# Kernel tuning notes

Hardware: AMD Instinct MI355X
Metric: run time of the kernel (lower is better)

Reference implementation:

```python
import jax, jax.numpy as jnp
import numpy as np

B, S, D = 2, 2048, 1024
H, DK = 16, 64
NUM_BUCKETS, MAX_DIST = 32, 128
EPS = 1e-6


def _relative_position_bucket(q_len, k_len):
    # T5 bidirectional relative position bucketing.
    ctx = jnp.arange(q_len)[:, None]
    mem = jnp.arange(k_len)[None, :]
    rel = mem - ctx  # [q, k]
    nb = NUM_BUCKETS // 2
    ret = (rel > 0).astype(jnp.int32) * nb
    n = jnp.abs(rel)
    max_exact = nb // 2
    is_small = n < max_exact
    n_safe = jnp.maximum(n, 1).astype(jnp.float32)
    val_large = max_exact + (
        jnp.log(n_safe / max_exact) / np.log(MAX_DIST / max_exact) * (nb - max_exact)
    ).astype(jnp.int32)
    val_large = jnp.minimum(val_large, nb - 1)
    return ret + jnp.where(is_small, n, val_large)  # [q, k] int32


def setup_inputs() -> dict:
    key = jax.random.key(0)
    ks = jax.random.split(key, 7)
    s = 0.02
    return {
        "hidden_states": jax.random.normal(ks[0], (B, S, D), jnp.float32),
        "ln_g": jnp.ones((D,), jnp.float32),
        "ln_b": jnp.zeros((D,), jnp.float32),
        "Wq": jax.random.normal(ks[1], (D, H * DK), jnp.float32) * s,
        "Wk": jax.random.normal(ks[2], (D, H * DK), jnp.float32) * s,
        "Wv": jax.random.normal(ks[3], (D, H * DK), jnp.float32) * s,
        "Wo": jax.random.normal(ks[4], (H * DK, D), jnp.float32) * s,
        "rel_bias": jax.random.normal(ks[5], (NUM_BUCKETS, H), jnp.float32) * s,
    }


def reference(hidden_states, ln_g, ln_b, Wq, Wk, Wv, Wo, rel_bias):
    b, s, d = hidden_states.shape
    # LayerNorm (nn.LayerNorm with affine, biased variance)
    mu = jnp.mean(hidden_states, axis=-1, keepdims=True)
    var = jnp.mean(jnp.square(hidden_states - mu), axis=-1, keepdims=True)
    normed = (hidden_states - mu) * jax.lax.rsqrt(var + EPS) * ln_g + ln_b
    # QKV projections (no bias), split heads
    q = (normed @ Wq).reshape(b, s, H, DK)
    k = (normed @ Wk).reshape(b, s, H, DK)
    v = (normed @ Wv).reshape(b, s, H, DK)
    # T5 attention: NO 1/sqrt(d) scaling; learned relative-position bias added to logits
    scores = jnp.einsum("bqhd,bkhd->bhqk", q, k)
    bucket = _relative_position_bucket(s, s)          # [s, s]
    bias = jnp.transpose(rel_bias[bucket], (2, 0, 1))  # [H, s, s]
    attn = jax.nn.softmax(scores + bias[None], axis=-1)
    ctx = jnp.einsum("bhqk,bkhd->bqhd", attn, v).reshape(b, s, H * DK)
    out = ctx @ Wo
    # residual (dropout is identity in eval)
    return hidden_states + out
```

## Files before the change

### kernel.cpp

```cpp
#include <hip/hip_runtime.h>
#include <hip/hip_bf16.h>
#include <math.h>

typedef __attribute__((__ext_vector_type__(8))) short bf16x8;
typedef __attribute__((__ext_vector_type__(4))) float f32x4;
typedef __attribute__((__ext_vector_type__(16))) float f32x16;
typedef __attribute__((__ext_vector_type__(4))) unsigned int u32x4;

#define B_ 2
#define S_ 2048
#define D_ 1024
#define H_ 16
#define DK_ 64
#define M_ (B_*S_)
#define N3_ 3072
#define BIAS_LEN 4096
#define M0_ 24.0f
#define L2E_ 1.4426950408889634f
#define KSTRIDE 66

__device__ __forceinline__ unsigned int cvtpk(float a, float b){
  unsigned int r;
  asm("v_cvt_pk_bf16_f32 %0, %1, %2" : "=v"(r) : "v"(a), "v"(b));
  return r;
}
__device__ __forceinline__ unsigned short f2bf(float f){
  unsigned int r;
  asm("v_cvt_pk_bf16_f32 %0, %1, %2" : "=v"(r) : "v"(f), "v"(f));
  return (unsigned short)r;
}
__device__ __forceinline__ float bf2f(unsigned short u){
  union{unsigned int i; float f;} v; v.i = ((unsigned int)u)<<16; return v.f;
}

__device__ __forceinline__ float fexp2(float x){
#if __has_builtin(__builtin_amdgcn_exp2f)
  return __builtin_amdgcn_exp2f(x);
#else
  return __expf(x * 0.6931471805599453f);
#endif
}

__device__ __forceinline__ f32x4 zero4(){
  f32x4 z; z[0]=0.f; z[1]=0.f; z[2]=0.f; z[3]=0.f; return z;
}

__device__ __forceinline__ f32x4 mfma16(bf16x8 a, bf16x8 b, f32x4 c){
  return __builtin_amdgcn_mfma_f32_16x16x32_bf16(a, b, c, 0, 0, 0);
}
__device__ __forceinline__ f32x16 mfma32(bf16x8 a, bf16x8 b, f32x16 c){
  return __builtin_amdgcn_mfma_f32_32x32x16_bf16(a, b, c, 0, 0, 0);
}

__device__ __forceinline__ void gload16(const void* g, void* l){
  __builtin_amdgcn_global_load_lds(
      (const __attribute__((address_space(1))) void*)g,
      (__attribute__((address_space(3))) void*)l, 16, 0, 0);
}

__global__ __launch_bounds__(256) void transpose_cast_kernel(
    const float* __restrict__ Wq, const float* __restrict__ Wk,
    const float* __restrict__ Wv, const float* __restrict__ Wo,
    unsigned short* __restrict__ Wcat_t, unsigned short* __restrict__ Wo_t)
{
  __shared__ float tile[64][65];
  const int k0 = blockIdx.x * 64;
  const int v0 = blockIdx.y * 64;
  const int sel = v0 >> 10;
  const float* W = (sel==0) ? Wq : (sel==1) ? Wk : (sel==2) ? Wv : Wo;
  const int nn0 = v0 & 1023;
  #pragma unroll
  for (int i=0;i<16;i++){
    int idx = i*256 + threadIdx.x;
    int r = idx >> 6, c = idx & 63;
    tile[r][c] = W[(size_t)(k0+r)*1024 + nn0 + c];
  }
  __syncthreads();
  #pragma unroll
  for (int i=0;i<16;i++){
    int idx = i*256 + threadIdx.x;
    int nr = idx >> 6, kc = idx & 63;
    unsigned short bv = f2bf(tile[kc][nr]);
    if (sel < 3) Wcat_t[(size_t)(v0+nr)*1024 + k0 + kc] = bv;
    else         Wo_t[(size_t)(v0-3072+nr)*1024 + k0 + kc] = bv;
  }
}

__global__ __launch_bounds__(256) void bias_tab_kernel(
    const float* __restrict__ rel_bias, float* __restrict__ biasTab)
{
  int t = blockIdx.x*256 + threadIdx.x;
  if (t >= H_*BIAS_LEN) return;
  int h = t / BIAS_LEN;
  int idx = t - h*BIAS_LEN;
  int rel = idx - (S_-1);
  int ret = (rel > 0) ? 16 : 0;
  int n = (rel < 0) ? -rel : rel;
  int bidx;
  if (n < 8) bidx = n;
  else {
    float vl = logf((float)n * 0.125f) / 2.7725887f * 8.0f;
    int v = 8 + (int)vl;
    bidx = (v < 15) ? v : 15;
  }
  biasTab[t] = (rel_bias[(ret + bidx)*H_ + h] - M0_) * L2E_;
}

__global__ __launch_bounds__(256) void ln_kernel(
    const float* __restrict__ x, const float* __restrict__ g,
    const float* __restrict__ bta, unsigned short* __restrict__ out)
{
  const int row = blockIdx.x;
  const int tid = threadIdx.x;
  float4 v = ((const float4*)(x + (size_t)row*D_))[tid];
  float s  = v.x+v.y+v.z+v.w;
  float ss = v.x*v.x+v.y*v.y+v.z*v.z+v.w*v.w;
  #pragma unroll
  for (int off=1; off<64; off<<=1){ s += __shfl_xor(s,off,64); ss += __shfl_xor(ss,off,64); }
  __shared__ float rs[4], rss[4];
  const int wid = tid >> 6, lane = tid & 63;
  if (lane == 0){ rs[wid] = s; rss[wid] = ss; }
  __syncthreads();
  s  = rs[0]+rs[1]+rs[2]+rs[3];
  ss = rss[0]+rss[1]+rss[2]+rss[3];
  float mu  = s * (1.0f/1024.0f);
  float var = ss * (1.0f/1024.0f) - mu*mu;
  float rstd = rsqrtf(var + 1e-6f);
  float4 gg = ((const float4*)g)[tid];
  float4 bb = ((const float4*)bta)[tid];
  uint2 o;
  o.x = cvtpk((v.x-mu)*rstd*gg.x + bb.x, (v.y-mu)*rstd*gg.y + bb.y);
  o.y = cvtpk((v.z-mu)*rstd*gg.z + bb.z, (v.w-mu)*rstd*gg.w + bb.w);
  ((uint2*)(out + (size_t)row*D_))[tid] = o;
}

__global__ __launch_bounds__(256) void gemm_qkv_kernel(
    const unsigned short* __restrict__ A,
    const unsigned short* __restrict__ Bt,
    unsigned short* __restrict__ Qb,
    unsigned short* __restrict__ Kb,
    unsigned short* __restrict__ Vtb)
{
  __shared__ unsigned short As[128*64];
  __shared__ unsigned short Bs[128*64];
  const int tid = threadIdx.x;
  const int wid = tid >> 6, lane = tid & 63;
  const int lr = lane & 15, lg = lane >> 4;
  const int wm = (wid >> 1) * 64, wn = (wid & 1) * 64;

  const int nbx = gridDim.x;
  const int total = nbx * gridDim.y;
  const int flat = blockIdx.y * nbx + blockIdx.x;
  const int swz = (flat & 7) * (total >> 3) + (flat >> 3);
  const int m0 = (swz % nbx) * 128, n0 = (swz / nbx) * 128;

  f32x4 acc[4][4];
  #pragma unroll
  for (int i=0;i<4;i++)
    #pragma unroll
    for (int j=0;j<4;j++) acc[i][j] = zero4();

  for (int k0 = 0; k0 < D_; k0 += 64) {
    __syncthreads();
    #pragma unroll
    for (int i=0;i<4;i++){
      int c = i*256 + tid;
      int row = c >> 3, ch = c & 7;
      int chs = ch ^ (row & 7);
      gload16(A  + (size_t)(m0+row)*D_ + k0 + chs*8, As + c*8);
      gload16(Bt + (size_t)(n0+row)*D_ + k0 + chs*8, Bs + c*8);
    }
    __syncthreads();
    #pragma unroll
    for (int kk=0;kk<2;kk++){
      bf16x8 aF[4], bF[4];
      #pragma unroll
      for (int mi=0;mi<4;mi++){
        int row = wm + mi*16 + lr;
        aF[mi] = *(const bf16x8*)&As[row*64 + (((kk*4+lg) ^ (row & 7)) * 8)];
      }
      #pragma unroll
      for (int ni=0;ni<4;ni++){
        int row = wn + ni*16 + lr;
        bF[ni] = *(const bf16x8*)&Bs[row*64 + (((kk*4+lg) ^ (row & 7)) * 8)];
      }
      #pragma unroll
      for (int mi=0;mi<4;mi++)
        #pragma unroll
        for (int ni=0;ni<4;ni++)
          acc[mi][ni] = mfma16(aF[mi], bF[ni], acc[mi][ni]);
    }
  }

  const int seln = n0 >> 10;
  if (seln == 2) {
    #pragma unroll
    for (int mi=0;mi<4;mi++)
      #pragma unroll
      for (int ni=0;ni<4;ni++){
        int m = m0 + wm + mi*16 + lg*4;
        int n = n0 + wn + ni*16 + lr;
        int nn = n & 1023, hh = nn >> 6, dk = nn & 63;
        int b = m >> 11, s = m & 2047;
        uint2 u;
        u.x = cvtpk(acc[mi][ni][0], acc[mi][ni][1]);
        u.y = cvtpk(acc[mi][ni][2], acc[mi][ni][3]);
        *(uint2*)(Vtb + (((size_t)(b*H_+hh))*DK_ + dk)*S_ + s) = u;
      }
  } else {
    unsigned short* __restrict__ dst = (seln == 0) ? Qb : Kb;
    #pragma unroll
    for (int mi=0;mi<4;mi++)
      #pragma unroll
      for (int ni=0;ni<4;ni++)
        #pragma unroll
        for (int r=0;r<4;r++){
          int m = m0 + wm + mi*16 + lg*4 + r;
          int n = n0 + wn + ni*16 + lr;
          int nn = n & 1023, hh = nn >> 6, dk = nn & 63;
          int b = m >> 11, s = m & 2047;
          dst[(((size_t)(b*H_+hh))*S_ + s)*DK_ + dk] = f2bf(acc[mi][ni][r]);
        }
  }
}

#define SOFTMAX_PV(Svec, BG, UNIP, UNIN, VF00, VF01, VF10, VF11, ACC, LS)        \
{                                                                                \
  float p[16];                                                                   \
  if (UNIP) {                                                                    \
    _Pragma("unroll")                                                            \
    for (int r=0;r<16;r++) p[r] = fexp2(__builtin_fmaf(Svec[r], L2E_, cpos));    \
  } else if (UNIN) {                                                             \
    _Pragma("unroll")                                                            \
    for (int r=0;r<16;r++) p[r] = fexp2(__builtin_fmaf(Svec[r], L2E_, cneg));    \
  } else {                                                                       \
    _Pragma("unroll")                                                            \
    for (int r=0;r<16;r++){                                                      \
      int key = k0 + st*32 + (r&3) + 8*(r>>2) + 4*hi;                            \
      p[r] = fexp2(__builtin_fmaf(Svec[r], L2E_, BG[key]));                      \
    }                                                                            \
  }                                                                              \
                                       \
  {                                                                              \
    float t0=p[0]+p[1], t1=p[2]+p[3], t2=p[4]+p[5], t3=p[6]+p[7];                \
    float t4=p[8]+p[9], t5=p[10]+p[11], t6=p[12]+p[13], t7=p[14]+p[15];          \
    LS += ((t0+t1)+(t2+t3)) + ((t4+t5)+(t6+t7));                                 \
  }                                                                              \
  unsigned int W00=cvtpk(p[0],p[1]),  W01=cvtpk(p[4],p[5]);                      \
  unsigned int W02=cvtpk(p[8],p[9]),  W03=cvtpk(p[12],p[13]);                    \
  unsigned int W10=cvtpk(p[2],p[3]),  W11=cvtpk(p[6],p[7]);                      \
  unsigned int W12=cvtpk(p[10],p[11]),W13=cvtpk(p[14],p[15]);                    \
  unsigned int X00=__shfl_xor(W00,32), X01=__shfl_xor(W01,32);                   \
  unsigned int X02=__shfl_xor(W02,32), X03=__shfl_xor(W03,32);                   \
  unsigned int X10=__shfl_xor(W10,32), X11=__shfl_xor(W11,32);                   \
  unsigned int X12=__shfl_xor(W12,32), X13=__shfl_xor(W13,32);                   \
  u32x4 pu0; u32x4 pu1;                                                          \
  pu0[0] = hi ? X01 : W00;  pu0[1] = hi ? X11 : W10;                             \
  pu0[2] = hi ? W01 : X00;  pu0[3] = hi ? W11 : X10;                             \
  pu1[0] = hi ? X03 : W02;  pu1[1] = hi ? X13 : W12;                             \
  pu1[2] = hi ? W03 : X02;  pu1[3] = hi ? W13 : X12;                             \
  bf16x8 pav0 = __builtin_bit_cast(bf16x8, pu0);                                 \
  bf16x8 pav1 = __builtin_bit_cast(bf16x8, pu1);                                 \
  ACC[0] = mfma32(pav0, VF00, ACC[0]);                                           \
  ACC[1] = mfma32(pav0, VF01, ACC[1]);                                           \
  ACC[0] = mfma32(pav1, VF10, ACC[0]);                                           \
  ACC[1] = mfma32(pav1, VF11, ACC[1]);                                           \
}

__global__ __launch_bounds__(256, 2) void attn_kernel(
    const unsigned short* __restrict__ Qb,
    const unsigned short* __restrict__ Kb,
    const unsigned short* __restrict__ Vtb,
    const float* __restrict__ biasTab,
    const float* __restrict__ rel_bias,
    unsigned short* __restrict__ Opart,
    float* __restrict__ Lpart)
{
  __shared__ unsigned short Ks[64*KSTRIDE];
  __shared__ unsigned short Vts[64*KSTRIDE];

  const int tid = threadIdx.x;
  const int wid = tid >> 6, lane = tid & 63;
  const int ql = lane & 31;
  const int hi = lane >> 5;

  const int flat = (blockIdx.z * 32 + blockIdx.y) * 8 + blockIdx.x;
  const int wf = (flat & 7) * 64 + (flat >> 3);
  const int qt = wf & 7;
  const int bh = (wf >> 3) & 31;
  const int kg = wf >> 8;

  const int h = bh & (H_-1);
  const int b = bh >> 4;
  const int kbase = kg << 10;
  const int q0w = qt*256 + wid*64;

  const float cpos = (rel_bias[31*H_ + h] - M0_) * L2E_;
  const float cneg = (rel_bias[15*H_ + h] - M0_) * L2E_;
  const float* bGa = biasTab + (size_t)h*BIAS_LEN + 2047 - (q0w + ql);
  const float* bGb = bGa - 32;

  const unsigned short* Qpa = Qb + ((size_t)bh*S_ + q0w + ql)*DK_;
  bf16x8 qfa[4], qfb[4];
  #pragma unroll
  for (int c=0;c<4;c++){
    qfa[c] = *(const bf16x8*)(Qpa + 16*c + 8*hi);
    qfb[c] = *(const bf16x8*)(Qpa + 32*DK_ + 16*c + 8*hi);
  }

  const unsigned short* Ksrc = Kb  + (size_t)bh*S_*DK_;
  const unsigned short* Vsrc = Vtb + (size_t)bh*DK_*S_;
  const int c0 = tid, c1 = tid + 256;
  const int r0 = c0 >> 3, ch0 = c0 & 7;
  const int r1 = c1 >> 3, ch1 = c1 & 7;

  f32x16 acca[2], accb[2];
  #pragma unroll
  for (int i=0;i<16;i++){ acca[0][i]=0.f; acca[1][i]=0.f; accb[0][i]=0.f; accb[1][i]=0.f; }
  float lsa = 0.f, lsb = 0.f;

  bf16x8 sk0 = *(const bf16x8*)(Ksrc + (size_t)(kbase + r0)*DK_ + ch0*8);
  bf16x8 sk1 = *(const bf16x8*)(Ksrc + (size_t)(kbase + r1)*DK_ + ch1*8);
  bf16x8 sv0 = *(const bf16x8*)(Vsrc + (size_t)r0*S_ + kbase + ch0*8);
  bf16x8 sv1 = *(const bf16x8*)(Vsrc + (size_t)r1*S_ + kbase + ch1*8);

  for (int k0 = kbase; k0 < kbase + 1024; k0 += 64) {
    __syncthreads();
    *(bf16x8*)&Ks [r0*KSTRIDE + ch0*8] = sk0;
    *(bf16x8*)&Ks [r1*KSTRIDE + ch1*8] = sk1;
    *(bf16x8*)&Vts[r0*KSTRIDE + ch0*8] = sv0;
    *(bf16x8*)&Vts[r1*KSTRIDE + ch1*8] = sv1;
    __syncthreads();
    if (k0 + 64 < kbase + 1024) {
      int kn = k0 + 64;
      sk0 = *(const bf16x8*)(Ksrc + (size_t)(kn + r0)*DK_ + ch0*8);
      sk1 = *(const bf16x8*)(Ksrc + (size_t)(kn + r1)*DK_ + ch1*8);
      sv0 = *(const bf16x8*)(Vsrc + (size_t)r0*S_ + kn + ch0*8);
      sv1 = *(const bf16x8*)(Vsrc + (size_t)r1*S_ + kn + ch1*8);
    }

    const bool upa = (k0 >= q0w + 122),      una = (k0 <= q0w - 154);
    const bool upb = (k0 >= q0w + 32 + 122), unb = (k0 <= q0w + 32 - 154);

    #pragma unroll
    for (int st=0; st<2; ++st){
      const int arow = st*32 + ql;
      bf16x8 kf0 = *(const bf16x8*)&Ks[arow*KSTRIDE + (0+hi)*8];
      bf16x8 kf1 = *(const bf16x8*)&Ks[arow*KSTRIDE + (2+hi)*8];
      bf16x8 kf2 = *(const bf16x8*)&Ks[arow*KSTRIDE + (4+hi)*8];
      bf16x8 kf3 = *(const bf16x8*)&Ks[arow*KSTRIDE + (6+hi)*8];

      f32x16 sa, sb;
      #pragma unroll
      for (int i=0;i<16;i++){ sa[i]=0.f; sb[i]=0.f; }
      sa = mfma32(kf0, qfa[0], sa); sb = mfma32(kf0, qfb[0], sb);
      sa = mfma32(kf1, qfa[1], sa); sb = mfma32(kf1, qfb[1], sb);
      sa = mfma32(kf2, qfa[2], sa); sb = mfma32(kf2, qfb[2], sb);
      sa = mfma32(kf3, qfa[3], sa); sb = mfma32(kf3, qfb[3], sb);

      bf16x8 vf00 = *(const bf16x8*)&Vts[(ql     )*KSTRIDE + (4*st+  hi)*8];
      bf16x8 vf01 = *(const bf16x8*)&Vts[(ql + 32)*KSTRIDE + (4*st+  hi)*8];
      bf16x8 vf10 = *(const bf16x8*)&Vts[(ql     )*KSTRIDE + (4*st+2+hi)*8];
      bf16x8 vf11 = *(const bf16x8*)&Vts[(ql + 32)*KSTRIDE + (4*st+2+hi)*8];

      SOFTMAX_PV(sa, bGa, upa, una, vf00, vf01, vf10, vf11, acca, lsa);
      SOFTMAX_PV(sb, bGb, upb, unb, vf00, vf01, vf10, vf11, accb, lsb);
    }
  }

  float lta = lsa + __shfl_xor(lsa, 32);
  float ltb = lsb + __shfl_xor(lsb, 32);
  if (hi == 0) {
    Lpart[((size_t)kg*B_*H_ + bh)*S_ + q0w + ql]      = lta;
    Lpart[((size_t)kg*B_*H_ + bh)*S_ + q0w + 32 + ql] = ltb;
  }
  #pragma unroll
  for (int r=0;r<16;r++){
    const int qr = (r&3) + 8*(r>>2) + 4*hi;
    #pragma unroll
    for (int dt=0; dt<2; ++dt){
      const int d = ql + 32*dt;
      Opart[(size_t)kg*M_*D_ + ((size_t)(b*S_ + q0w + qr)*H_ + h)*DK_ + d]      = f2bf(acca[dt][r]);
      Opart[(size_t)kg*M_*D_ + ((size_t)(b*S_ + q0w + 32 + qr)*H_ + h)*DK_ + d] = f2bf(accb[dt][r]);
    }
  }
}

__global__ __launch_bounds__(256) void gemm_out_kernel(
    const unsigned short* __restrict__ Opart,
    const float* __restrict__ Lpart,
    const unsigned short* __restrict__ Wo_t,
    const float* __restrict__ resid,
    float* __restrict__ outf)
{
  __shared__ unsigned short As[64*64];
  __shared__ unsigned short Bs[128*64];
  const int tid = threadIdx.x;
  const int wid = tid >> 6, lane = tid & 63;
  const int lr = lane & 15, lg = lane >> 4;
  const int wm = (wid & 1) * 32, wn = (wid >> 1) * 64;

  const int nbx = gridDim.x;
  const int total = nbx * gridDim.y;
  const int flat = blockIdx.y * nbx + blockIdx.x;
  const int swz = (flat & 7) * (total >> 3) + (flat >> 3);
  const int m0 = (swz % nbx) * 64, n0 = (swz / nbx) * 128;

  f32x4 acc[2][4];
  #pragma unroll
  for (int i=0;i<2;i++)
    #pragma unroll
    for (int j=0;j<4;j++) acc[i][j] = zero4();

  for (int k0 = 0; k0 < D_; k0 += 64) {
    const int hh = k0 >> 6;
    __syncthreads();
    #pragma unroll
    for (int i=0;i<4;i++){
      int c = i*256 + tid;
      int row = c >> 3, ch = c & 7;
      int chs = ch ^ (row & 7);
      gload16(Wo_t + (size_t)(n0+row)*D_ + k0 + chs*8, Bs + c*8);
    }
    #pragma unroll
    for (int i=0;i<2;i++){
      int c = i*256 + tid;
      int row = c >> 3, ch = c & 7;
      int m = m0 + row;
      int bb = m >> 11, s = m & 2047;
      int bhh = bb*H_ + hh;
      float l0 = Lpart[(size_t)bhh*S_ + s];
      float l1 = Lpart[(size_t)B_*H_*S_ + (size_t)bhh*S_ + s];
      float li = 1.0f / (l0 + l1);
      size_t addr = (size_t)m*D_ + k0 + ch*8;
      bf16x8 p0 = *(const bf16x8*)(Opart + addr);
      bf16x8 p1 = *(const bf16x8*)(Opart + (size_t)M_*D_ + addr);
      u32x4 o;
      #pragma unroll
      for (int j=0;j<4;j++){
        float a = (bf2f((unsigned short)p0[2*j+0]) + bf2f((unsigned short)p1[2*j+0])) * li;
        float cc= (bf2f((unsigned short)p0[2*j+1]) + bf2f((unsigned short)p1[2*j+1])) * li;
        o[j] = cvtpk(a, cc);
      }
      *(u32x4*)&As[row*64 + ((ch ^ (row & 7))*8)] = o;
    }
    __syncthreads();
    #pragma unroll
    for (int kk=0;kk<2;kk++){
      bf16x8 aF[2], bF[4];
      #pragma unroll
      for (int mi=0;mi<2;mi++){
        int row = wm + mi*16 + lr;
        aF[mi] = *(const bf16x8*)&As[row*64 + (((kk*4+lg) ^ (row & 7)) * 8)];
      }
      #pragma unroll
      for (int ni=0;ni<4;ni++){
        int row = wn + ni*16 + lr;
        bF[ni] = *(const bf16x8*)&Bs[row*64 + (((kk*4+lg) ^ (row & 7)) * 8)];
      }
      #pragma unroll
      for (int mi=0;mi<2;mi++)
        #pragma unroll
        for (int ni=0;ni<4;ni++)
          acc[mi][ni] = mfma16(aF[mi], bF[ni], acc[mi][ni]);
    }
  }

  #pragma unroll
  for (int mi=0;mi<2;mi++)
    #pragma unroll
    for (int ni=0;ni<4;ni++)
      #pragma unroll
      for (int r=0;r<4;r++){
        int m = m0 + wm + mi*16 + lg*4 + r;
        int n = n0 + wn + ni*16 + lr;
        outf[(size_t)m*D_ + n] = acc[mi][ni][r] + resid[(size_t)m*D_ + n];
      }
}

extern "C" void kernel_launch(void* const* d_in, const int* in_sizes, int n_in,
                              void* d_out, int out_size, void* d_ws, size_t ws_size,
                              hipStream_t stream) {
  const float* hidden   = (const float*)d_in[0];
  const float* ln_g     = (const float*)d_in[1];
  const float* ln_b     = (const float*)d_in[2];
  const float* Wq       = (const float*)d_in[3];
  const float* Wk       = (const float*)d_in[4];
  const float* Wv       = (const float*)d_in[5];
  const float* Wo       = (const float*)d_in[6];
  const float* rel_bias = (const float*)d_in[7];
  float* out = (float*)d_out;

  char* ws = (char*)d_ws;
  const size_t off_ln   = 0;
  const size_t off_wcat = 8388608;
  const size_t off_q    = 16777216;
  const size_t off_k    = 25165824;
  const size_t off_vt   = 33554432;
  const size_t off_bias = 50331648;
  const size_t off_lp   = 50593792;
  const size_t off_wo   = 51118080;

  unsigned short* ln_out  = (unsigned short*)(ws + off_ln);
  unsigned short* Wcat_t  = (unsigned short*)(ws + off_wcat);
  unsigned short* Wo_t    = (unsigned short*)(ws + off_wo);
  unsigned short* Qb      = (unsigned short*)(ws + off_q);
  unsigned short* Kb      = (unsigned short*)(ws + off_k);
  unsigned short* Vtb     = (unsigned short*)(ws + off_vt);
  float*          biasTab = (float*)(ws + off_bias);
  float*          Lpart   = (float*)(ws + off_lp);
  unsigned short* Opart   = (unsigned short*)(ws + 0);

  transpose_cast_kernel<<<dim3(16,64), 256, 0, stream>>>(Wq, Wk, Wv, Wo, Wcat_t, Wo_t);
  bias_tab_kernel<<<(H_*BIAS_LEN + 255)/256, 256, 0, stream>>>(rel_bias, biasTab);
  ln_kernel<<<M_, 256, 0, stream>>>(hidden, ln_g, ln_b, ln_out);
  gemm_qkv_kernel<<<dim3(M_/128, N3_/128), 256, 0, stream>>>(
      ln_out, Wcat_t, Qb, Kb, Vtb);
  attn_kernel<<<dim3(8, 32, 2), 256, 0, stream>>>(
      Qb, Kb, Vtb, biasTab, rel_bias, Opart, Lpart);
  gemm_out_kernel<<<dim3(M_/64, D_/128), 256, 0, stream>>>(
      Opart, Lpart, Wo_t, hidden, out);
}
```

Baseline: 140.6 us.

## Double-buffer K/V in LDS and optionally split attention keys four ways

Attention now keeps two LDS buffers for K and V tiles. The next tile is written while the current one is consumed, so each iteration needs one barrier instead of two. The key dimension split is templated: if the workspace is large enough, it uses four key partitions (double the blocks) and gemm_out sums four partials. This adds more partial-output traffic in bf16 and relies on ws_size to choose the path.

```diff
diff --git a/kernel.cpp b/kernel.cpp
--- a/kernel.cpp
+++ b/kernel.cpp
@@ -267,6 +267,7 @@
   ACC[1] = mfma32(pav1, VF11, ACC[1]);                                           \
 }
 
+template<int NS>
 __global__ __launch_bounds__(256, 2) void attn_kernel(
     const unsigned short* __restrict__ Qb,
     const unsigned short* __restrict__ Kb,
@@ -276,8 +277,10 @@
     unsigned short* __restrict__ Opart,
     float* __restrict__ Lpart)
 {
-  __shared__ unsigned short Ks[64*KSTRIDE];
-  __shared__ unsigned short Vts[64*KSTRIDE];
+  __shared__ unsigned short Ks[2][64*KSTRIDE];
+  __shared__ unsigned short Vts[2][64*KSTRIDE];
+  constexpr int NT = (S_/NS)/64;
+  constexpr int KSPAN = S_/NS;
 
   const int tid = threadIdx.x;
   const int wid = tid >> 6, lane = tid & 63;
@@ -285,14 +288,14 @@
   const int hi = lane >> 5;
 
   const int flat = (blockIdx.z * 32 + blockIdx.y) * 8 + blockIdx.x;
-  const int wf = (flat & 7) * 64 + (flat >> 3);
+  const int wf = (flat & 7) * (32 * NS) + (flat >> 3);
   const int qt = wf & 7;
   const int bh = (wf >> 3) & 31;
   const int kg = wf >> 8;
 
   const int h = bh & (H_-1);
   const int b = bh >> 4;
-  const int kbase = kg << 10;
+  const int kbase = kg * KSPAN;
   const int q0w = qt*256 + wid*64;
 
   const float cpos = (rel_bias[31*H_ + h] - M0_) * L2E_;
@@ -323,21 +326,24 @@
   bf16x8 sk1 = *(const bf16x8*)(Ksrc + (size_t)(kbase + r1)*DK_ + ch1*8);
   bf16x8 sv0 = *(const bf16x8*)(Vsrc + (size_t)r0*S_ + kbase + ch0*8);
   bf16x8 sv1 = *(const bf16x8*)(Vsrc + (size_t)r1*S_ + kbase + ch1*8);
-
-  for (int k0 = kbase; k0 < kbase + 1024; k0 += 64) {
-    __syncthreads();
-    *(bf16x8*)&Ks [r0*KSTRIDE + ch0*8] = sk0;
-    *(bf16x8*)&Ks [r1*KSTRIDE + ch1*8] = sk1;
-    *(bf16x8*)&Vts[r0*KSTRIDE + ch0*8] = sv0;
-    *(bf16x8*)&Vts[r1*KSTRIDE + ch1*8] = sv1;
-    __syncthreads();
-    if (k0 + 64 < kbase + 1024) {
+  *(bf16x8*)&Ks [0][r0*KSTRIDE + ch0*8] = sk0;
+  *(bf16x8*)&Ks [0][r1*KSTRIDE + ch1*8] = sk1;
+  *(bf16x8*)&Vts[0][r0*KSTRIDE + ch0*8] = sv0;
+  *(bf16x8*)&Vts[0][r1*KSTRIDE + ch1*8] = sv1;
+  __syncthreads();
+
+  for (int t = 0; t < NT; ++t) {
+    const int k0 = kbase + t*64;
+    const int cur = t & 1;
+    if (t + 1 < NT) {
       int kn = k0 + 64;
       sk0 = *(const bf16x8*)(Ksrc + (size_t)(kn + r0)*DK_ + ch0*8);
       sk1 = *(const bf16x8*)(Ksrc + (size_t)(kn + r1)*DK_ + ch1*8);
       sv0 = *(const bf16x8*)(Vsrc + (size_t)r0*S_ + kn + ch0*8);
       sv1 = *(const bf16x8*)(Vsrc + (size_t)r1*S_ + kn + ch1*8);
     }
+    const unsigned short* Ksb  = Ks[cur];
+    const unsigned short* Vtsb = Vts[cur];
 
     const bool upa = (k0 >= q0w + 122),      una = (k0 <= q0w - 154);
     const bool upb = (k0 >= q0w + 32 + 122), unb = (k0 <= q0w + 32 - 154);
@@ -345,10 +351,10 @@
     #pragma unroll
     for (int st=0; st<2; ++st){
       const int arow = st*32 + ql;
-      bf16x8 kf0 = *(const bf16x8*)&Ks[arow*KSTRIDE + (0+hi)*8];
-      bf16x8 kf1 = *(const bf16x8*)&Ks[arow*KSTRIDE + (2+hi)*8];
-      bf16x8 kf2 = *(const bf16x8*)&Ks[arow*KSTRIDE + (4+hi)*8];
-      bf16x8 kf3 = *(const bf16x8*)&Ks[arow*KSTRIDE + (6+hi)*8];
+      bf16x8 kf0 = *(const bf16x8*)&Ksb[arow*KSTRIDE + (0+hi)*8];
+      bf16x8 kf1 = *(const bf16x8*)&Ksb[arow*KSTRIDE + (2+hi)*8];
+      bf16x8 kf2 = *(const bf16x8*)&Ksb[arow*KSTRIDE + (4+hi)*8];
+      bf16x8 kf3 = *(const bf16x8*)&Ksb[arow*KSTRIDE + (6+hi)*8];
 
       f32x16 sa, sb;
       #pragma unroll
@@ -358,14 +364,23 @@
       sa = mfma32(kf2, qfa[2], sa); sb = mfma32(kf2, qfb[2], sb);
       sa = mfma32(kf3, qfa[3], sa); sb = mfma32(kf3, qfb[3], sb);
 
-      bf16x8 vf00 = *(const bf16x8*)&Vts[(ql     )*KSTRIDE + (4*st+  hi)*8];
-      bf16x8 vf01 = *(const bf16x8*)&Vts[(ql + 32)*KSTRIDE + (4*st+  hi)*8];
-      bf16x8 vf10 = *(const bf16x8*)&Vts[(ql     )*KSTRIDE + (4*st+2+hi)*8];
-      bf16x8 vf11 = *(const bf16x8*)&Vts[(ql + 32)*KSTRIDE + (4*st+2+hi)*8];
+      bf16x8 vf00 = *(const bf16x8*)&Vtsb[(ql     )*KSTRIDE + (4*st+  hi)*8];
+      bf16x8 vf01 = *(const bf16x8*)&Vtsb[(ql + 32)*KSTRIDE + (4*st+  hi)*8];
+      bf16x8 vf10 = *(const bf16x8*)&Vtsb[(ql     )*KSTRIDE + (4*st+2+hi)*8];
+      bf16x8 vf11 = *(const bf16x8*)&Vtsb[(ql + 32)*KSTRIDE + (4*st+2+hi)*8];
 
       SOFTMAX_PV(sa, bGa, upa, una, vf00, vf01, vf10, vf11, acca, lsa);
       SOFTMAX_PV(sb, bGb, upb, unb, vf00, vf01, vf10, vf11, accb, lsb);
     }
+
+    if (t + 1 < NT) {
+      const int nxt = cur ^ 1;
+      *(bf16x8*)&Ks [nxt][r0*KSTRIDE + ch0*8] = sk0;
+      *(bf16x8*)&Ks [nxt][r1*KSTRIDE + ch1*8] = sk1;
+      *(bf16x8*)&Vts[nxt][r0*KSTRIDE + ch0*8] = sv0;
+      *(bf16x8*)&Vts[nxt][r1*KSTRIDE + ch1*8] = sv1;
+    }
+    __syncthreads();
   }
 
   float lta = lsa + __shfl_xor(lsa, 32);
@@ -386,6 +401,7 @@
   }
 }
 
+template<int NS>
 __global__ __launch_bounds__(256) void gemm_out_kernel(
     const unsigned short* __restrict__ Opart,
     const float* __restrict__ Lpart,
@@ -429,19 +445,23 @@
       int m = m0 + row;
       int bb = m >> 11, s = m & 2047;
       int bhh = bb*H_ + hh;
-      float l0 = Lpart[(size_t)bhh*S_ + s];
-      float l1 = Lpart[(size_t)B_*H_*S_ + (size_t)bhh*S_ + s];
-      float li = 1.0f / (l0 + l1);
+      float lsum = 0.f;
+      #pragma unroll
+      for (int s2=0;s2<NS;s2++) lsum += Lpart[((size_t)s2*B_*H_ + bhh)*S_ + s];
+      float li = 1.0f / lsum;
       size_t addr = (size_t)m*D_ + k0 + ch*8;
-      bf16x8 p0 = *(const bf16x8*)(Opart + addr);
-      bf16x8 p1 = *(const bf16x8*)(Opart + (size_t)M_*D_ + addr);
+      float va[8];
+      #pragma unroll
+      for (int j=0;j<8;j++) va[j] = 0.f;
+      #pragma unroll
+      for (int s2=0;s2<NS;s2++){
+        bf16x8 p = *(const bf16x8*)(Opart + (size_t)s2*M_*D_ + addr);
+        #pragma unroll
+        for (int j=0;j<8;j++) va[j] += bf2f((unsigned short)p[j]);
+      }
       u32x4 o;
       #pragma unroll
-      for (int j=0;j<4;j++){
-        float a = (bf2f((unsigned short)p0[2*j+0]) + bf2f((unsigned short)p1[2*j+0])) * li;
-        float cc= (bf2f((unsigned short)p0[2*j+1]) + bf2f((unsigned short)p1[2*j+1])) * li;
-        o[j] = cvtpk(a, cc);
-      }
+      for (int j=0;j<4;j++) o[j] = cvtpk(va[2*j]*li, va[2*j+1]*li);
       *(u32x4*)&As[row*64 + ((ch ^ (row & 7))*8)] = o;
     }
     __syncthreads();
@@ -492,17 +512,28 @@
   float* out = (float*)d_out;
 
   char* ws = (char*)d_ws;
-  const size_t off_ln   = 0;
-  const size_t off_wcat = 8388608;
-  const size_t off_q    = 16777216;
-  const size_t off_k    = 25165824;
-  const size_t off_vt   = 33554432;
-  const size_t off_bias = 50331648;
-  const size_t off_lp   = 50593792;
-  const size_t off_wo   = 51118080;
-
-  unsigned short* ln_out  = (unsigned short*)(ws + off_ln);
-  unsigned short* Wcat_t  = (unsigned short*)(ws + off_wcat);
+  const size_t SZP = (size_t)M_*D_*2;
+  const bool split4 = ws_size >= 62128128ULL;
+
+  size_t off_q, off_k, off_vt, off_bias, off_lp, off_wo;
+  if (split4) {
+    off_q    = 33554432;
+    off_k    = 41943040;
+    off_vt   = 50331648;
+    off_bias = 58720256;
+    off_lp   = 58982400;
+    off_wo   = 60030976;
+  } else {
+    off_q    = 16777216;
+    off_k    = 25165824;
+    off_vt   = 33554432;
+    off_bias = 50331648;
+    off_lp   = 50593792;
+    off_wo   = 51118080;
+  }
+
+  unsigned short* ln_out  = (unsigned short*)(ws + 0);
+  unsigned short* Wcat_t  = (unsigned short*)(ws + SZP);
   unsigned short* Wo_t    = (unsigned short*)(ws + off_wo);
   unsigned short* Qb      = (unsigned short*)(ws + off_q);
   unsigned short* Kb      = (unsigned short*)(ws + off_k);
@@ -516,8 +547,15 @@
   ln_kernel<<<M_, 256, 0, stream>>>(hidden, ln_g, ln_b, ln_out);
   gemm_qkv_kernel<<<dim3(M_/128, N3_/128), 256, 0, stream>>>(
       ln_out, Wcat_t, Qb, Kb, Vtb);
-  attn_kernel<<<dim3(8, 32, 2), 256, 0, stream>>>(
-      Qb, Kb, Vtb, biasTab, rel_bias, Opart, Lpart);
-  gemm_out_kernel<<<dim3(M_/64, D_/128), 256, 0, stream>>>(
-      Opart, Lpart, Wo_t, hidden, out);
-}
+  if (split4) {
+    attn_kernel<4><<<dim3(8, 32, 4), 256, 0, stream>>>(
+        Qb, Kb, Vtb, biasTab, rel_bias, Opart, Lpart);
+    gemm_out_kernel<4><<<dim3(M_/64, D_/128), 256, 0, stream>>>(
+        Opart, Lpart, Wo_t, hidden, out);
+  } else {
+    attn_kernel<2><<<dim3(8, 32, 2), 256, 0, stream>>>(
+        Qb, Kb, Vtb, biasTab, rel_bias, Opart, Lpart);
+    gemm_out_kernel<2><<<dim3(M_/64, D_/128), 256, 0, stream>>>(
+        Opart, Lpart, Wo_t, hidden, out);
+  }
+}
```

Result: slower. 194.7 us (+38.4%).
